# Kernel tuning notes

Hardware: AMD Instinct MI355X
Metric: run time of the kernel (lower is better)

## Reference

```python
import jax, jax.numpy as jnp
import numpy as np

B = 131072          # batch size
D = 128             # input_dim
OUT = 64            # output_dim
L = 32              # number of masked (CustomizedLinear) layers = hidden + output nodes


def setup_inputs() -> dict:
    key = jax.random.key(0)
    ks = jax.random.split(key, 8)
    x = jax.random.normal(ks[0], (B, D), dtype=jnp.float32)
    # start_node: nn.Linear(D, D)
    w_start = jax.random.normal(ks[1], (D, D), dtype=jnp.float32) / np.sqrt(D)
    b_start = jnp.zeros((D,), dtype=jnp.float32)
    # masked linear layers: weight elementwise-multiplied by binary graph mask
    raw_w = jax.random.normal(ks[2], (L, D, D), dtype=jnp.float32) / np.sqrt(D)
    mask = (jax.random.uniform(ks[3], (L, D, D)) < 0.25).astype(jnp.float32)
    masked_w = raw_w * mask          # [L, D, D]
    layer_b = jnp.zeros((L, D), dtype=jnp.float32)
    # output_layer: nn.Linear(D, OUT)
    w_out = jax.random.normal(ks[4], (OUT, D), dtype=jnp.float32) / np.sqrt(D)
    b_out = jnp.zeros((OUT,), dtype=jnp.float32)
    return {"x": x, "w_start": w_start, "b_start": b_start,
            "masked_w": masked_w, "layer_b": layer_b,
            "w_out": w_out, "b_out": b_out}


def reference(x, w_start, b_start, masked_w, layer_b, w_out, b_out):
    # x = start_node(x)
    x0 = x @ w_start.T + b_start          # [B, D]

    # sequential masked-linear chain with relu + residual back to x0
    def step(h, params):
        w, b = params                      # w: [D, D], b: [D]
        h = jax.nn.relu(h @ w.T + b) + x0  # x_ = relu(layer(x_)) + x
        return h, None

    h, _ = jax.lax.scan(step, x0, (masked_w, layer_b))

    logits = h @ w_out.T + b_out          # [B, OUT]
    return jax.nn.softmax(logits, axis=1)
```

## Files before the change

### kernel.cpp

```cpp
#include <hip/hip_runtime.h>
#include <hip/hip_bf16.h>
#include <stdint.h>


typedef short bs8 __attribute__((ext_vector_type(8)));
typedef float f32x4 __attribute__((ext_vector_type(4)));

union Frag { bs8 v; uint32_t u[4]; };
union F4   { float4 f; f32x4 v; };

__device__ __forceinline__ uint32_t cvtpk(float lo, float hi) {
#if __has_builtin(__builtin_amdgcn_cvt_pk_bf16_f32)
  auto r = __builtin_amdgcn_cvt_pk_bf16_f32(lo, hi);
  uint32_t u; __builtin_memcpy(&u, &r, 4);
  return u;
#else
  union { float f; uint32_t u; } a, b; a.f = lo; b.f = hi;
  uint32_t ra = a.u + 0x7fffu + ((a.u >> 16) & 1u);
  uint32_t rb = b.u + 0x7fffu + ((b.u >> 16) & 1u);
  return (ra >> 16) | (rb & 0xffff0000u);
#endif
}

__global__ void prep_frags(const float* __restrict__ w_start,
                           const float* __restrict__ b_start,
                           const float* __restrict__ masked_w,
                           const float* __restrict__ layer_b,
                           const float* __restrict__ w_out,
                           const float* __restrict__ b_out,
                           uint16_t* __restrict__ dst) {
  int t = blockIdx.x * 256 + threadIdx.x;
  if (t >= 69680) return;
  if (t >= 68608) {
    int f = (t - 68608) * 4;
    int c, off; const float* src;
    if (f < 128)       { c = f >> 6;               off = f & 63; src = b_start + f; }
    else if (f < 4224) { int g = f - 128;  c = 2 + (g >> 6); off = g & 63; src = layer_b + g; }
    else               { int g = f - 4224; c = 66;           off = g;      src = b_out + g; }
    float4 v = *reinterpret_cast<const float4*>(src);
    *reinterpret_cast<float4*>(
        reinterpret_cast<float*>(dst + (size_t)c * 8320 + 8192) + off) = v;
    return;
  }
  int lane = t & 63, kt = (t >> 6) & 3, q = lane >> 4, m15 = lane & 15;
  float f[8];
  int c, ntloc;
  if (t < 2048) {
    int nt = (t >> 8) & 7;
    c = nt >> 2; ntloc = nt & 3;
    const float* s = w_start + (nt * 16 + m15) * 128 + q * 8 + kt * 32;
    #pragma unroll
    for (int j = 0; j < 8; ++j) f[j] = s[j];
  } else if (t < 67584) {
    int t2 = t - 2048, l = t2 >> 11, nt = (t2 >> 8) & 7;
    c = 2 + 2 * l + (nt >> 2); ntloc = nt & 3;
    const float* s = masked_w + ((l * 128) + nt * 16 + m15) * 128 + q * 4 + kt * 32;
    #pragma unroll
    for (int j = 0; j < 8; ++j) f[j] = s[(j & 3) + 16 * (j >> 2)];
  } else {
    int t3 = t - 67584, nt = (t3 >> 8) & 3;
    c = 66; ntloc = nt;
    const float* s = w_out + (nt * 16 + m15) * 128 + q * 4 + kt * 32;
    #pragma unroll
    for (int j = 0; j < 8; ++j) f[j] = s[(j & 3) + 16 * (j >> 2)];
  }
  uint4 o;
  o.x = cvtpk(f[0], f[1]); o.y = cvtpk(f[2], f[3]);
  o.z = cvtpk(f[4], f[5]); o.w = cvtpk(f[6], f[7]);
  *reinterpret_cast<uint4*>(dst + (size_t)c * 8320 +
                            ((ntloc * 4 + kt) * 64 + lane) * 8) = o;
}

extern __shared__ uint16_t lds[];

#define VMW(N) asm volatile("s_waitcnt vmcnt(" #N ")" ::: "memory")

__global__ void __launch_bounds__(256, 3)
wann_main(const float* __restrict__ x,
          const uint16_t* __restrict__ wfrag,
          float* __restrict__ out) {
  const int tid  = threadIdx.x;
  const int lane = tid & 63;
  const int wave = tid >> 6;
  const int q    = lane >> 4;
  const int mc   = lane & 15;
  const long batch0 = (long)blockIdx.x * 128 + wave * 32;
  const f32x4 zero4 = {0.f, 0.f, 0.f, 0.f};

  auto slotp = [&](uint32_t s) -> uint16_t* { return lds + (size_t)s * 8320; };

  auto stage = [&](uint16_t* dstb, uint32_t c) {
    const uint16_t* srcb = wfrag + (size_t)c * 8320;
    #pragma unroll
    for (int i = 0; i < 4; ++i) {
      __builtin_amdgcn_global_load_lds(
          (const __attribute__((address_space(1))) void*)(srcb + i * 2048 + wave * 512 + lane * 8),
          (__attribute__((address_space(3))) void*)(dstb + i * 2048 + wave * 512),
          16, 0, 0);
    }
    __builtin_amdgcn_global_load_lds(
        (const __attribute__((address_space(1))) void*)(srcb + 8192 + lane * 2),
        (__attribute__((address_space(3))) void*)(dstb + 8192),
        4, 0, 0);
  };

  auto barx = [&]() {
    asm volatile("" ::: "memory");
    __builtin_amdgcn_s_barrier();
    asm volatile("" ::: "memory");
  };

  Frag xf[2][4];
  #pragma unroll
  for (int mt = 0; mt < 2; ++mt) {
    const float* xrow = x + (batch0 + mt * 16 + mc) * 128 + q * 8;
    #pragma unroll
    for (int kt = 0; kt < 4; ++kt) {
      float4 a = *reinterpret_cast<const float4*>(xrow + kt * 32);
      float4 b = *reinterpret_cast<const float4*>(xrow + kt * 32 + 4);
      xf[mt][kt].u[0] = cvtpk(a.x, a.y);
      xf[mt][kt].u[1] = cvtpk(a.z, a.w);
      xf[mt][kt].u[2] = cvtpk(b.x, b.y);
      xf[mt][kt].u[3] = cvtpk(b.z, b.w);
    }
  }

  stage(slotp(0), 0);
  stage(slotp(1), 1);

  Frag x0f[2][4], hA[2][4], hB[2][4];

  auto start_half = [&](const uint16_t* buf, int h) {
    const float* bbb = reinterpret_cast<const float*>(buf + 8192);
    #pragma unroll
    for (int pp = 0; pp < 2; ++pp) {
      const int p = 2 * h + pp;
      F4 bb[2];
      #pragma unroll
      for (int ntl = 0; ntl < 2; ++ntl)
        bb[ntl].f = *reinterpret_cast<const float4*>(bbb + (2 * pp + ntl) * 16 + q * 4);
      f32x4 acc[2][2];
      __builtin_amdgcn_s_setprio(1);
      #pragma unroll
      for (int kt = 0; kt < 4; ++kt)
        #pragma unroll
        for (int ntl = 0; ntl < 2; ++ntl) {
          const int ntloc = 2 * pp + ntl;
          Frag wf;
          wf.v = *reinterpret_cast<const bs8*>(buf + ((ntloc * 4 + kt) * 64 + lane) * 8);
          #pragma unroll
          for (int mt = 0; mt < 2; ++mt) {
            f32x4 c = (kt == 0) ? bb[ntl].v : acc[ntl][mt];
            acc[ntl][mt] = __builtin_amdgcn_mfma_f32_16x16x32_bf16(wf.v, xf[mt][kt].v, c, 0, 0, 0);
          }
        }
      __builtin_amdgcn_s_setprio(0);
      #pragma unroll
      for (int mt = 0; mt < 2; ++mt)
        #pragma unroll
        for (int ntl = 0; ntl < 2; ++ntl) {
          x0f[mt][p].u[2 * ntl + 0] = cvtpk(acc[ntl][mt][0], acc[ntl][mt][1]);
          x0f[mt][p].u[2 * ntl + 1] = cvtpk(acc[ntl][mt][2], acc[ntl][mt][3]);
        }
    }
  };

  auto chain_half = [&](const uint16_t* buf, int h,
                        Frag (&hin)[2][4], Frag (&hout)[2][4]) {
    const float* bbb = reinterpret_cast<const float*>(buf + 8192);
    #pragma unroll
    for (int pp = 0; pp < 2; ++pp) {
      const int p = 2 * h + pp;
      F4 bb[2];
      #pragma unroll
      for (int ntl = 0; ntl < 2; ++ntl)
        bb[ntl].f = *reinterpret_cast<const float4*>(bbb + (2 * pp + ntl) * 16 + q * 4);
      f32x4 acc[2][2];
      __builtin_amdgcn_s_setprio(1);
      #pragma unroll
      for (int kt = 0; kt < 4; ++kt)
        #pragma unroll
        for (int ntl = 0; ntl < 2; ++ntl) {
          const int ntloc = 2 * pp + ntl;
          Frag wf;
          wf.v = *reinterpret_cast<const bs8*>(buf + ((ntloc * 4 + kt) * 64 + lane) * 8);
          #pragma unroll
          for (int mt = 0; mt < 2; ++mt) {
            f32x4 c = (kt == 0) ? bb[ntl].v : acc[ntl][mt];
            acc[ntl][mt] = __builtin_amdgcn_mfma_f32_16x16x32_bf16(wf.v, hin[mt][kt].v, c, 0, 0, 0);
          }
        }
      __builtin_amdgcn_s_setprio(0);
      #pragma unroll
      for (int mt = 0; mt < 2; ++mt)
        #pragma unroll
        for (int ntl = 0; ntl < 2; ++ntl) {
          f32x4 r = __builtin_elementwise_max(acc[ntl][mt], zero4);
          uint32_t xw0 = x0f[mt][p].u[2 * ntl + 0];
          uint32_t xw1 = x0f[mt][p].u[2 * ntl + 1];
          f32x4 xv;
          xv[0] = __uint_as_float(xw0 << 16);
          xv[1] = __uint_as_float(xw0 & 0xffff0000u);
          xv[2] = __uint_as_float(xw1 << 16);
          xv[3] = __uint_as_float(xw1 & 0xffff0000u);
          r = r + xv;
          hout[mt][p].u[2 * ntl + 0] = cvtpk(r[0], r[1]);
          hout[mt][p].u[2 * ntl + 1] = cvtpk(r[2], r[3]);
        }
    }
  };

  VMW(5); barx(); stage(slotp(2), 2);
  start_half(slotp(0), 0);
  VMW(5); barx(); stage(slotp(0), 3);
  start_half(slotp(1), 1);
  #pragma unroll
  for (int mt = 0; mt < 2; ++mt)
    #pragma unroll
    for (int kt = 0; kt < 4; ++kt)
      hA[mt][kt].v = x0f[mt][kt].v;

  uint32_t s0 = 2;
  #pragma unroll 1
  for (int l = 0; l < 32; l += 2) {
    const uint32_t s1 = (s0 + 1 < 3) ? s0 + 1 : 0;
    const uint32_t s2 = (s1 + 1 < 3) ? s1 + 1 : 0;
    const uint32_t c0 = 2 + 2 * (uint32_t)l;

    VMW(5); barx(); stage(slotp(s2), c0 + 2);
    chain_half(slotp(s0), 0, hA, hB);
    VMW(5); barx(); stage(slotp(s0), c0 + 3);
    chain_half(slotp(s1), 1, hA, hB);
    VMW(5); barx(); if (c0 + 4 <= 66) stage(slotp(s1), c0 + 4);
    chain_half(slotp(s2), 0, hB, hA);
    VMW(5); barx(); if (c0 + 5 <= 66) stage(slotp(s2), c0 + 5);
    chain_half(slotp(s0), 1, hB, hA);

    s0 = s1;
  }

  VMW(0); barx();
  const uint16_t* wo = slotp(0);
  const float* bob = reinterpret_cast<const float*>(wo + 8192);
  F4 bo[4];
  #pragma unroll
  for (int nt = 0; nt < 4; ++nt)
    bo[nt].f = *reinterpret_cast<const float4*>(bob + nt * 16 + q * 4);
  f32x4 ao[4][2];
  __builtin_amdgcn_s_setprio(1);
  #pragma unroll
  for (int kt = 0; kt < 4; ++kt) {
    #pragma unroll
    for (int nt = 0; nt < 4; ++nt) {
      Frag wf;
      wf.v = *reinterpret_cast<const bs8*>(wo + ((nt * 4 + kt) * 64 + lane) * 8);
      #pragma unroll
      for (int mt = 0; mt < 2; ++mt) {
        f32x4 c = (kt == 0) ? bo[nt].v : ao[nt][mt];
        ao[nt][mt] = __builtin_amdgcn_mfma_f32_16x16x32_bf16(wf.v, hA[mt][kt].v, c, 0, 0, 0);
      }
    }
  }
  __builtin_amdgcn_s_setprio(0);

  float* tr = reinterpret_cast<float*>(reinterpret_cast<char*>(lds) + 16640)
              + wave * 1088;
  #pragma unroll
  for (int mt = 0; mt < 2; ++mt) {
    float e[16];
    float M = -3.0e38f;
    #pragma unroll
    for (int nt = 0; nt < 4; ++nt)
      #pragma unroll
      for (int r = 0; r < 4; ++r)
        M = fmaxf(M, ao[nt][mt][r]);
    M = fmaxf(M, __shfl_xor(M, 16, 64));
    M = fmaxf(M, __shfl_xor(M, 32, 64));
    float S = 0.0f;
    #pragma unroll
    for (int nt = 0; nt < 4; ++nt)
      #pragma unroll
      for (int r = 0; r < 4; ++r) {
        float t = exp2f((ao[nt][mt][r] - M) * 1.4426950408889634f);
        e[nt * 4 + r] = t;
        S += t;
      }
    S += __shfl_xor(S, 16, 64);
    S += __shfl_xor(S, 32, 64);
    const float inv = 1.0f / S;
    #pragma unroll
    for (int nt = 0; nt < 4; ++nt) {
      float4 pv;
      pv.x = e[nt * 4 + 0] * inv;
      pv.y = e[nt * 4 + 1] * inv;
      pv.z = e[nt * 4 + 2] * inv;
      pv.w = e[nt * 4 + 3] * inv;
      *reinterpret_cast<float4*>(tr + mc * 68 + nt * 16 + q * 4) = pv;
    }
    __asm__ volatile("s_waitcnt lgkmcnt(0)" ::: "memory");
    #pragma unroll
    for (int it = 0; it < 4; ++it) {
      int row = it * 4 + (lane >> 4);
      float4 v = *reinterpret_cast<const float4*>(tr + row * 68 + (lane & 15) * 4);
      long gr = batch0 + mt * 16 + row;
      *reinterpret_cast<float4*>(out + gr * 64 + (lane & 15) * 4) = v;
    }
    __asm__ volatile("s_waitcnt lgkmcnt(0)" ::: "memory");
  }
}

extern "C" void kernel_launch(void* const* d_in, const int* in_sizes, int n_in,
                              void* d_out, int out_size, void* d_ws, size_t ws_size,
                              hipStream_t stream) {
  const float* x        = (const float*)d_in[0];
  const float* w_start  = (const float*)d_in[1];
  const float* b_start  = (const float*)d_in[2];
  const float* masked_w = (const float*)d_in[3];
  const float* layer_b  = (const float*)d_in[4];
  const float* w_out    = (const float*)d_in[5];
  const float* b_out    = (const float*)d_in[6];
  uint16_t* wfrag = (uint16_t*)d_ws;

  prep_frags<<<273, 256, 0, stream>>>(w_start, b_start, masked_w, layer_b,
                                      w_out, b_out, wfrag);
  wann_main<<<1024, 256, 49920, stream>>>(x, wfrag, (float*)d_out);
}
```

Before: 270.2 us.

## Use 512-thread blocks sharing staged weight slots and shrink MFMA accumulator live set

Doubles the block to 8 waves covering 256 batch rows, so each staged weight layer in LDS is reused by twice as many rows and per-wave global-to-LDS copy work is halved (vmcnt waits adjusted accordingly). The chain loops are reordered to compute one output tile at a time, which lowers accumulator register pressure to suit the tighter launch bounds. The softmax transpose scratch now reuses the weight slot region after an extra barrier, so 8 waves fit in the same LDS allocation. Risks are fewer resident blocks if registers spill, and barriers that now synchronise more waves.

```diff
diff --git a/kernel.cpp b/kernel.cpp
--- a/kernel.cpp
+++ b/kernel.cpp
@@ -75,7 +75,7 @@
 
 #define VMW(N) asm volatile("s_waitcnt vmcnt(" #N ")" ::: "memory")
 
-__global__ void __launch_bounds__(256, 3)
+__global__ void __launch_bounds__(512, 4)
 wann_main(const float* __restrict__ x,
           const uint16_t* __restrict__ wfrag,
           float* __restrict__ out) {
@@ -84,7 +84,7 @@
   const int wave = tid >> 6;
   const int q    = lane >> 4;
   const int mc   = lane & 15;
-  const long batch0 = (long)blockIdx.x * 128 + wave * 32;
+  const long batch0 = (long)blockIdx.x * 256 + wave * 32;
   const f32x4 zero4 = {0.f, 0.f, 0.f, 0.f};
 
   auto slotp = [&](uint32_t s) -> uint16_t* { return lds + (size_t)s * 8320; };
@@ -92,10 +92,10 @@
   auto stage = [&](uint16_t* dstb, uint32_t c) {
     const uint16_t* srcb = wfrag + (size_t)c * 8320;
     #pragma unroll
-    for (int i = 0; i < 4; ++i) {
+    for (int i = 0; i < 2; ++i) {
       __builtin_amdgcn_global_load_lds(
-          (const __attribute__((address_space(1))) void*)(srcb + i * 2048 + wave * 512 + lane * 8),
-          (__attribute__((address_space(3))) void*)(dstb + i * 2048 + wave * 512),
+          (const __attribute__((address_space(1))) void*)(srcb + wave * 1024 + i * 512 + lane * 8),
+          (__attribute__((address_space(3))) void*)(dstb + wave * 1024 + i * 512),
           16, 0, 0);
     }
     __builtin_amdgcn_global_load_lds(
@@ -135,33 +135,30 @@
     #pragma unroll
     for (int pp = 0; pp < 2; ++pp) {
       const int p = 2 * h + pp;
-      F4 bb[2];
-      #pragma unroll
-      for (int ntl = 0; ntl < 2; ++ntl)
-        bb[ntl].f = *reinterpret_cast<const float4*>(bbb + (2 * pp + ntl) * 16 + q * 4);
-      f32x4 acc[2][2];
-      __builtin_amdgcn_s_setprio(1);
-      #pragma unroll
-      for (int kt = 0; kt < 4; ++kt)
+      #pragma unroll
+      for (int ntl = 0; ntl < 2; ++ntl) {
+        const int ntloc = 2 * pp + ntl;
+        F4 bb;
+        bb.f = *reinterpret_cast<const float4*>(bbb + ntloc * 16 + q * 4);
+        f32x4 acc[2];
+        __builtin_amdgcn_s_setprio(1);
         #pragma unroll
-        for (int ntl = 0; ntl < 2; ++ntl) {
-          const int ntloc = 2 * pp + ntl;
+        for (int kt = 0; kt < 4; ++kt) {
           Frag wf;
           wf.v = *reinterpret_cast<const bs8*>(buf + ((ntloc * 4 + kt) * 64 + lane) * 8);
           #pragma unroll
           for (int mt = 0; mt < 2; ++mt) {
-            f32x4 c = (kt == 0) ? bb[ntl].v : acc[ntl][mt];
-            acc[ntl][mt] = __builtin_amdgcn_mfma_f32_16x16x32_bf16(wf.v, xf[mt][kt].v, c, 0, 0, 0);
+            f32x4 c = (kt == 0) ? bb.v : acc[mt];
+            acc[mt] = __builtin_amdgcn_mfma_f32_16x16x32_bf16(wf.v, xf[mt][kt].v, c, 0, 0, 0);
           }
         }
-      __builtin_amdgcn_s_setprio(0);
-      #pragma unroll
-      for (int mt = 0; mt < 2; ++mt)
+        __builtin_amdgcn_s_setprio(0);
         #pragma unroll
-        for (int ntl = 0; ntl < 2; ++ntl) {
-          x0f[mt][p].u[2 * ntl + 0] = cvtpk(acc[ntl][mt][0], acc[ntl][mt][1]);
-          x0f[mt][p].u[2 * ntl + 1] = cvtpk(acc[ntl][mt][2], acc[ntl][mt][3]);
+        for (int mt = 0; mt < 2; ++mt) {
+          x0f[mt][p].u[2 * ntl + 0] = cvtpk(acc[mt][0], acc[mt][1]);
+          x0f[mt][p].u[2 * ntl + 1] = cvtpk(acc[mt][2], acc[mt][3]);
         }
+      }
     }
   };
 
@@ -171,31 +168,27 @@
     #pragma unroll
     for (int pp = 0; pp < 2; ++pp) {
       const int p = 2 * h + pp;
-      F4 bb[2];
-      #pragma unroll
-      for (int ntl = 0; ntl < 2; ++ntl)
-        bb[ntl].f = *reinterpret_cast<const float4*>(bbb + (2 * pp + ntl) * 16 + q * 4);
-      f32x4 acc[2][2];
-      __builtin_amdgcn_s_setprio(1);
-      #pragma unroll
-      for (int kt = 0; kt < 4; ++kt)
+      #pragma unroll
+      for (int ntl = 0; ntl < 2; ++ntl) {
+        const int ntloc = 2 * pp + ntl;
+        F4 bb;
+        bb.f = *reinterpret_cast<const float4*>(bbb + ntloc * 16 + q * 4);
+        f32x4 acc[2];
+        __builtin_amdgcn_s_setprio(1);
         #pragma unroll
-        for (int ntl = 0; ntl < 2; ++ntl) {
-          const int ntloc = 2 * pp + ntl;
+        for (int kt = 0; kt < 4; ++kt) {
           Frag wf;
           wf.v = *reinterpret_cast<const bs8*>(buf + ((ntloc * 4 + kt) * 64 + lane) * 8);
           #pragma unroll
           for (int mt = 0; mt < 2; ++mt) {
-            f32x4 c = (kt == 0) ? bb[ntl].v : acc[ntl][mt];
-            acc[ntl][mt] = __builtin_amdgcn_mfma_f32_16x16x32_bf16(wf.v, hin[mt][kt].v, c, 0, 0, 0);
+            f32x4 c = (kt == 0) ? bb.v : acc[mt];
+            acc[mt] = __builtin_amdgcn_mfma_f32_16x16x32_bf16(wf.v, hin[mt][kt].v, c, 0, 0, 0);
           }
         }
-      __builtin_amdgcn_s_setprio(0);
-      #pragma unroll
-      for (int mt = 0; mt < 2; ++mt)
+        __builtin_amdgcn_s_setprio(0);
         #pragma unroll
-        for (int ntl = 0; ntl < 2; ++ntl) {
-          f32x4 r = __builtin_elementwise_max(acc[ntl][mt], zero4);
+        for (int mt = 0; mt < 2; ++mt) {
+          f32x4 r = __builtin_elementwise_max(acc[mt], zero4);
           uint32_t xw0 = x0f[mt][p].u[2 * ntl + 0];
           uint32_t xw1 = x0f[mt][p].u[2 * ntl + 1];
           f32x4 xv;
@@ -207,12 +200,13 @@
           hout[mt][p].u[2 * ntl + 0] = cvtpk(r[0], r[1]);
           hout[mt][p].u[2 * ntl + 1] = cvtpk(r[2], r[3]);
         }
+      }
     }
   };
 
-  VMW(5); barx(); stage(slotp(2), 2);
+  VMW(3); barx(); stage(slotp(2), 2);
   start_half(slotp(0), 0);
-  VMW(5); barx(); stage(slotp(0), 3);
+  VMW(3); barx(); stage(slotp(0), 3);
   start_half(slotp(1), 1);
   #pragma unroll
   for (int mt = 0; mt < 2; ++mt)
@@ -227,13 +221,13 @@
     const uint32_t s2 = (s1 + 1 < 3) ? s1 + 1 : 0;
     const uint32_t c0 = 2 + 2 * (uint32_t)l;
 
-    VMW(5); barx(); stage(slotp(s2), c0 + 2);
+    VMW(3); barx(); stage(slotp(s2), c0 + 2);
     chain_half(slotp(s0), 0, hA, hB);
-    VMW(5); barx(); stage(slotp(s0), c0 + 3);
+    VMW(3); barx(); stage(slotp(s0), c0 + 3);
     chain_half(slotp(s1), 1, hA, hB);
-    VMW(5); barx(); if (c0 + 4 <= 66) stage(slotp(s1), c0 + 4);
+    VMW(3); barx(); if (c0 + 4 <= 66) stage(slotp(s1), c0 + 4);
     chain_half(slotp(s2), 0, hB, hA);
-    VMW(5); barx(); if (c0 + 5 <= 66) stage(slotp(s2), c0 + 5);
+    VMW(3); barx(); if (c0 + 5 <= 66) stage(slotp(s2), c0 + 5);
     chain_half(slotp(s0), 1, hB, hA);
 
     s0 = s1;
@@ -263,8 +257,8 @@
   }
   __builtin_amdgcn_s_setprio(0);
 
-  float* tr = reinterpret_cast<float*>(reinterpret_cast<char*>(lds) + 16640)
-              + wave * 1088;
+  barx();
+  float* tr = reinterpret_cast<float*>(lds) + wave * 1088;
   #pragma unroll
   for (int mt = 0; mt < 2; ++mt) {
     float e[16];
@@ -323,5 +317,5 @@
 
   prep_frags<<<273, 256, 0, stream>>>(w_start, b_start, masked_w, layer_b,
                                       w_out, b_out, wfrag);
-  wann_main<<<1024, 256, 49920, stream>>>(x, wfrag, (float*)d_out);
+  wann_main<<<512, 512, 49920, stream>>>(x, wfrag, (float*)d_out);
 }
```

Result: slower. 356.1 us (+31.8%).
